# Kernel tuning notes

Hardware: AMD Instinct MI355X
Metric: run time of the kernel (lower is better)

## Reference

```python
import jax, jax.numpy as jnp
import numpy as np

B = 32768
IN = 2
H = 512
OUT = 1
OM = 128   # output_module_size
HG = 128   # halt_gate_size
MAX_ITER = 32
EPS = 1e-3


def _w(k, shape, fan_in):
    bound = 1.0 / np.sqrt(fan_in)
    return jax.random.uniform(k, shape, jnp.float32, -bound, bound)


def setup_inputs() -> dict:
    key = jax.random.key(0)
    ks = jax.random.split(key, 32)
    d = {"x": jax.random.normal(ks[0], (B, IN), jnp.float32)}
    # four LSTM gates: input Linear(IN,H) and hidden Linear(H,H), each with bias
    names = ["i", "f", "c", "o"]
    for j, g in enumerate(names):
        d[f"W{g}_x"] = _w(ks[1 + 4 * j], (IN, H), IN)
        d[f"b{g}_x"] = _w(ks[2 + 4 * j], (H,), IN)
        d[f"W{g}_h"] = _w(ks[3 + 4 * j], (H, H), H)
        d[f"b{g}_h"] = _w(ks[4 + 4 * j], (H,), H)
    # halt gate: Linear(H,HG) -> ReLU -> Linear(HG,1) -> Sigmoid
    d["halt_W1"] = _w(ks[17], (H, HG), H)
    d["halt_b1"] = _w(ks[18], (HG,), H)
    d["halt_W2"] = _w(ks[19], (HG, 1), HG)
    d["halt_b2"] = _w(ks[20], (1,), HG)
    # output module: Linear(H,OM) -> ReLU -> Linear(OM,OM) -> Linear(OM,OUT) -> Sigmoid
    d["out_W1"] = _w(ks[21], (H, OM), H)
    d["out_b1"] = _w(ks[22], (OM,), H)
    d["out_W2"] = _w(ks[23], (OM, OM), OM)
    d["out_b2"] = _w(ks[24], (OM,), OM)
    d["out_W3"] = _w(ks[25], (OM, OUT), OM)
    d["out_b3"] = _w(ks[26], (OUT,), OM)
    return d


def _act_forward(x, Wi_x, bi_x, Wi_h, bi_h, Wf_x, bf_x, Wf_h, bf_h,
                 Wc_x, bc_x, Wc_h, bc_h, Wo_x, bo_x, Wo_h, bo_h,
                 halt_W1, halt_b1, halt_W2, halt_b2,
                 out_W1, out_b1, out_W2, out_b2, out_W3, out_b3):
    b = x.shape[0]
    # input projections are iteration-invariant: precompute once
    xi = x @ Wi_x + bi_x
    xf = x @ Wf_x + bf_x
    xc = x @ Wc_x + bc_x
    xo = x @ Wo_x + bo_x

    def step(carry, t):
        state, cell, p_sum, active, acc = carry
        i_g = jax.nn.sigmoid(xi + state @ Wi_h + bi_h)
        f_g = jax.nn.sigmoid(xf + state @ Wf_h + bf_h)
        c_g = jnp.tanh(xc + state @ Wc_h + bc_h)
        o_g = jax.nn.sigmoid(xo + state @ Wo_h + bo_h)
        am = active[:, None]
        new_cell = jnp.where(am, f_g * cell + i_g * c_g, cell)
        new_state = jnp.where(am, o_g * jnp.tanh(new_cell), state)
        # output head (inactive rows contribute zero weight below)
        h1 = jax.nn.relu(new_state @ out_W1 + out_b1)
        out = jax.nn.sigmoid((h1 @ out_W2 + out_b2) @ out_W3 + out_b3)  # [B,OUT]
        # halt probability
        hh = jax.nn.relu(new_state @ halt_W1 + halt_b1)
        halt = jax.nn.sigmoid(hh @ halt_W2 + halt_b2)[:, 0]  # [B]
        halt = jnp.where(active, halt, 0.0)
        p_new = p_sum + halt
        is_last = t == (MAX_ITER - 1)
        finished = (p_new >= 1.0 - EPS) | is_last
        adj = active & finished
        halt_adj = jnp.where(adj, halt + (1.0 - p_new), halt)
        p_new = jnp.where(adj, 1.0, p_new)
        acc = acc + out * halt_adj[:, None]
        active_new = active & jnp.logical_not(finished)
        return (new_state, new_cell, p_new, active_new, acc), None

    init = (
        jnp.zeros((b, H), jnp.float32),   # state
        jnp.zeros((b, H), jnp.float32),   # cell
        jnp.zeros((b,), jnp.float32),     # p_sum
        jnp.ones((b,), bool),             # active
        jnp.zeros((b, OUT), jnp.float32), # weighted-output accumulator
    )
    (state, cell, p_sum, active, acc), _ = jax.lax.scan(step, init, jnp.arange(MAX_ITER))
    return acc


def reference(x, Wi_x, bi_x, Wi_h, bi_h, Wf_x, bf_x, Wf_h, bf_h,
              Wc_x, bc_x, Wc_h, bc_h, Wo_x, bo_x, Wo_h, bo_h,
              halt_W1, halt_b1, halt_W2, halt_b2,
              out_W1, out_b1, out_W2, out_b2, out_W3, out_b3):
    return _act_forward(x, Wi_x, bi_x, Wi_h, bi_h, Wf_x, bf_x, Wf_h, bf_h,
                        Wc_x, bc_x, Wc_h, bc_h, Wo_x, bo_x, Wo_h, bo_h,
                        halt_W1, halt_b1, halt_W2, halt_b2,
                        out_W1, out_b1, out_W2, out_b2, out_W3, out_b3)
```

## Files before the change

kernel.cpp:

```cpp
#include <hip/hip_runtime.h>
#include <hip/hip_bf16.h>

#define KD   544
#define ASTR 552
#define RPB  64
#define THR  512
#define T1   3
#define NROW 32768

typedef __bf16 bf8 __attribute__((ext_vector_type(8)));
typedef float f32x4 __attribute__((ext_vector_type(4)));

__device__ __forceinline__ float sigm(float x)  { return 1.0f / (1.0f + __expf(-x)); }
__device__ __forceinline__ float tanh_(float x) { return 2.0f / (1.0f + __expf(-2.0f * x)) - 1.0f; }

__global__ void pack_all(const float* __restrict__ Wi_h, const float* __restrict__ Wf_h,
                         const float* __restrict__ Wc_h, const float* __restrict__ Wo_h,
                         const float* __restrict__ Wi_x, const float* __restrict__ Wf_x,
                         const float* __restrict__ Wc_x, const float* __restrict__ Wo_x,
                         const float* __restrict__ bi_x, const float* __restrict__ bf_x,
                         const float* __restrict__ bc_x, const float* __restrict__ bo_x,
                         const float* __restrict__ bi_h, const float* __restrict__ bf_h,
                         const float* __restrict__ bc_h, const float* __restrict__ bo_h,
                         const float* __restrict__ outW1, const float* __restrict__ outb1,
                         const float* __restrict__ haltW1, const float* __restrict__ haltb1,
                         const float* __restrict__ outW2, const float* __restrict__ outb2,
                         const float* __restrict__ outW3, const float* __restrict__ outb3,
                         __bf16* __restrict__ whT, __bf16* __restrict__ w1cat,
                         float* __restrict__ w23, float* __restrict__ b23,
                         int* __restrict__ cntp)
{
  __shared__ float tile[64][65];
  const int b = blockIdx.x;
  const int tid = threadIdx.x;

  if (b < 256) {
    const int g = b >> 6, ct = (b >> 3) & 7, kt = b & 7;
    const int c0 = ct * 64, k0 = kt * 64;
    const float* Wh = (g == 0) ? Wi_h : (g == 1) ? Wf_h : (g == 2) ? Wc_h : Wo_h;
    const int ty = tid >> 6, tx = tid & 63;
#pragma unroll
    for (int r = 0; r < 16; ++r) {
      int kl = r * 4 + ty;
      tile[kl][tx] = Wh[(size_t)(k0 + kl) * 512 + c0 + tx];
    }
    __syncthreads();
    const int jj = tid >> 2, kq = tid & 3;
    bf8 lo, hi;
#pragma unroll
    for (int i = 0; i < 8; ++i) lo[i] = (__bf16)tile[kq * 16 + i][jj];
#pragma unroll
    for (int i = 0; i < 8; ++i) hi[i] = (__bf16)tile[kq * 16 + 8 + i][jj];
    __bf16* dst = whT + (size_t)(g * 512 + c0 + jj) * KD + k0 + kq * 16;
    *(bf8*)dst = lo;
    *(bf8*)(dst + 8) = hi;
  } else if (b < 288) {
    const int b2 = b - 256;
    const int g = b2 >> 3, ct = b2 & 7;
    const float* Wx = (g == 0) ? Wi_x : (g == 1) ? Wf_x : (g == 2) ? Wc_x : Wo_x;
    const float* bx = (g == 0) ? bi_x : (g == 1) ? bf_x : (g == 2) ? bc_x : bo_x;
    const float* bh = (g == 0) ? bi_h : (g == 1) ? bf_h : (g == 2) ? bc_h : bo_h;
    const int jj = tid >> 2, kq = tid & 3;
    const int c = ct * 64 + jj;
    bf8 v;
#pragma unroll
    for (int i = 0; i < 8; ++i) {
      int k = 512 + kq * 8 + i;
      float f = 0.0f;
      if (k == 512)      f = Wx[c];
      else if (k == 513) f = Wx[512 + c];
      else if (k == 514) f = bx[c] + bh[c];
      v[i] = (__bf16)f;
    }
    *(bf8*)(whT + (size_t)(g * 512 + c) * KD + 512 + kq * 8) = v;
  } else if (b < 320) {
    const int b2 = b - 288;
    const int src = b2 >> 4, jt = (b2 >> 3) & 1, kt = b2 & 7;
    const float* W = src ? haltW1 : outW1;
    const int c0 = jt * 64, k0 = kt * 64;
    const int ty = tid >> 6, tx = tid & 63;
#pragma unroll
    for (int r = 0; r < 16; ++r) {
      int kl = r * 4 + ty;
      tile[kl][tx] = W[(size_t)(k0 + kl) * 128 + c0 + tx];
    }
    __syncthreads();
    const int jj = tid >> 2, kq = tid & 3;
    bf8 lo, hi;
#pragma unroll
    for (int i = 0; i < 8; ++i) lo[i] = (__bf16)tile[kq * 16 + i][jj];
#pragma unroll
    for (int i = 0; i < 8; ++i) hi[i] = (__bf16)tile[kq * 16 + 8 + i][jj];
    __bf16* dst = w1cat + (size_t)(src * 128 + c0 + jj) * KD + k0 + kq * 16;
    *(bf8*)dst = lo;
    *(bf8*)(dst + 8) = hi;
  } else if (b < 324) {
    const int b2 = b - 320;
    const int jj = tid >> 2, kq = tid & 3;
    const int j = b2 * 64 + jj;
    const float bias = (j < 128) ? outb1[j] : haltb1[j - 128];
    bf8 v;
#pragma unroll
    for (int i = 0; i < 8; ++i) {
      int k = 512 + kq * 8 + i;
      v[i] = (__bf16)((k == 514) ? bias : 0.0f);
    }
    *(bf8*)(w1cat + (size_t)j * KD + 512 + kq * 8) = v;
  } else {
    const int c1 = tid;
    if (c1 < 128) {
      float s = 0.0f;
      for (int c2 = 0; c2 < 128; ++c2) s += outW2[c1 * 128 + c2] * outW3[c2];
      w23[c1] = s;
    }
    if (c1 == 0) {
      float bb = 0.0f;
      for (int c2 = 0; c2 < 128; ++c2) bb += outb2[c2] * outW3[c2];
      b23[0] = bb + outb3[0];
      cntp[0] = 0;
    }
  }
}

template<bool P1>
__global__ __launch_bounds__(THR, 2) void act_pass(
    const float* __restrict__ x,
    const __bf16* __restrict__ whT,
    const __bf16* __restrict__ w1cat,
    const float* __restrict__ w23,
    const float* __restrict__ b23p,
    const float* __restrict__ haltW2,
    const float* __restrict__ haltb2,
    __bf16* __restrict__ sstate,
    __bf16* __restrict__ scell,
    float* __restrict__ spsum,
    float* __restrict__ saccum,
    int* __restrict__ sidx,
    int* __restrict__ cntp,
    float* __restrict__ out)
{
  int cnt_v = 0, sbase = 0;
  if constexpr (!P1) {
    cnt_v = cntp[0];
    sbase = blockIdx.x * RPB;
    if (sbase >= cnt_v) return;
  }

  __shared__ __align__(16) __bf16 Abuf[2][RPB][ASTR];
  __shared__ float wv[256];
  __shared__ float partials[8][RPB];
  __shared__ int anyact_s;
  __shared__ int rowslot[RPB];

  const int tid  = threadIdx.x;
  const int wave = tid >> 6;
  const int lane = tid & 63;
  const int lg   = lane >> 4;
  const int lc   = lane & 15;
  const int row0 = blockIdx.x * RPB;

  if (tid < 256) wv[tid] = (tid < 128) ? w23[tid] : haltW2[tid - 128];

  if constexpr (P1) {
    for (int w = tid; w < 2 * RPB * 69; w += THR) {
      int bb  = w / (RPB * 69);
      int rem = w - bb * (RPB * 69);
      int r   = rem / 69;
      int j   = rem - r * 69;
      bf8 v;
#pragma unroll
      for (int e = 0; e < 8; ++e) v[e] = (__bf16)0.0f;
      if (j == 64) {
        v[0] = (__bf16)x[(row0 + r) * 2 + 0];
        v[1] = (__bf16)x[(row0 + r) * 2 + 1];
        v[2] = (__bf16)1.0f;
      }
      *(bf8*)&Abuf[bb][r][j * 8] = v;
    }
  } else {
    for (int w = tid; w < RPB * 68; w += THR) {
      int r = w / 68, j = w - r * 68;
      int slot = sbase + r;
      bf8 v;
#pragma unroll
      for (int e = 0; e < 8; ++e) v[e] = (__bf16)0.0f;
      if (slot < cnt_v) v = *(const bf8*)(sstate + (size_t)slot * KD + j * 8);
      *(bf8*)&Abuf[0][r][j * 8] = v;
      if (j >= 64) *(bf8*)&Abuf[1][r][j * 8] = v;
    }
    for (int w = tid; w < RPB * 64; w += THR) {
      int r = w / 64, j = w - r * 64;
      int slot = sbase + r;
      bf8 v;
#pragma unroll
      for (int e = 0; e < 8; ++e) v[e] = (__bf16)0.0f;
      if (slot < cnt_v) v = *(const bf8*)(scell + (size_t)slot * 512 + j * 8);
      *(bf8*)&Abuf[1][r][j * 8] = v;
    }
  }
  if (tid == 0) anyact_s = 1;
  __syncthreads();

  float cell[4][4][4];
  if constexpr (P1) {
#pragma unroll
    for (int n = 0; n < 4; ++n)
#pragma unroll
      for (int m = 0; m < 4; ++m)
#pragma unroll
        for (int q = 0; q < 4; ++q) cell[n][m][q] = 0.0f;
  } else {
#pragma unroll
    for (int n = 0; n < 4; ++n)
#pragma unroll
      for (int m = 0; m < 4; ++m)
#pragma unroll
        for (int q = 0; q < 4; ++q)
          cell[n][m][q] = (float)Abuf[1][m * 16 + lg * 4 + q][wave * 64 + n * 16 + lc];
  }

  bool  valid, active;
  float p_sum, accum;
  int   oidx;
  if constexpr (P1) {
    valid = (tid < 64); active = valid;
    p_sum = 0.0f; accum = 0.0f; oidx = row0 + tid;
  } else {
    int slot = sbase + tid;
    valid = (tid < 64) && (slot < cnt_v);
    active = valid;
    p_sum = valid ? spsum[slot]  : 1.0f;
    accum = valid ? saccum[slot] : 0.0f;
    oidx  = valid ? sidx[slot]   : 0;
    __syncthreads();
  }

  const float b23 = b23p[0];
  const float bh2 = haltb2[0];
  const f32x4 zero4 = {0.0f, 0.0f, 0.0f, 0.0f};

  int cur = 0;
  const int T0 = P1 ? 0 : T1;
  const int TE = P1 ? T1 : 32;
  for (int t = T0; t < TE; ++t) {
    const int kstart = (P1 && t == 0) ? 16 : 0;
#pragma unroll
    for (int n = 0; n < 4; ++n) {
      const int colb = wave * 64 + n * 16 + lc;
      const __bf16* bp[4];
      bp[0] = whT + (size_t)colb * KD + lg * 8;
      bp[1] = bp[0] + (size_t)512  * KD;
      bp[2] = bp[0] + (size_t)1024 * KD;
      bp[3] = bp[0] + (size_t)1536 * KD;
      f32x4 acc[4][4];
#pragma unroll
      for (int g = 0; g < 4; ++g)
#pragma unroll
        for (int m = 0; m < 4; ++m) acc[g][m] = zero4;

      bf8 bA[4], bB[4], avA[4];
      const int k1 = (kstart < 16) ? kstart + 1 : 16;
#pragma unroll
      for (int g = 0; g < 4; ++g) {
        bA[g] = *(const bf8*)(bp[g] + kstart * 32);
        bB[g] = *(const bf8*)(bp[g] + k1 * 32);
      }
#pragma unroll
      for (int m = 0; m < 4; ++m)
        avA[m] = *(const bf8*)&Abuf[cur][m * 16 + lc][kstart * 32 + lg * 8];

#pragma unroll 1
      for (int kk = kstart; kk <= 16; ++kk) {
        const int kp2 = (kk + 2 <= 16) ? kk + 2 : 16;
        const int kp1 = (kk + 1 <= 16) ? kk + 1 : 16;
        bf8 bC[4], avB[4];
#pragma unroll
        for (int g = 0; g < 4; ++g) bC[g] = *(const bf8*)(bp[g] + kp2 * 32);
#pragma unroll
        for (int m = 0; m < 4; ++m)
          avB[m] = *(const bf8*)&Abuf[cur][m * 16 + lc][kp1 * 32 + lg * 8];
#pragma unroll
        for (int m = 0; m < 4; ++m) {
          acc[0][m] = __builtin_amdgcn_mfma_f32_16x16x32_bf16(avA[m], bA[0], acc[0][m], 0, 0, 0);
          acc[1][m] = __builtin_amdgcn_mfma_f32_16x16x32_bf16(avA[m], bA[1], acc[1][m], 0, 0, 0);
          acc[2][m] = __builtin_amdgcn_mfma_f32_16x16x32_bf16(avA[m], bA[2], acc[2][m], 0, 0, 0);
          acc[3][m] = __builtin_amdgcn_mfma_f32_16x16x32_bf16(avA[m], bA[3], acc[3][m], 0, 0, 0);
        }
#pragma unroll
        for (int g = 0; g < 4; ++g) { bA[g] = bB[g]; bB[g] = bC[g]; }
#pragma unroll
        for (int m = 0; m < 4; ++m) avA[m] = avB[m];
      }
#pragma unroll
      for (int m = 0; m < 4; ++m) {
#pragma unroll
        for (int q = 0; q < 4; ++q) {
          float iv = sigm(acc[0][m][q]);
          float fv = sigm(acc[1][m][q]);
          float cv = tanh_(acc[2][m][q]);
          float ov = sigm(acc[3][m][q]);
          float cn = fv * cell[n][m][q] + iv * cv;
          cell[n][m][q] = cn;
          float h = ov * tanh_(cn);
          Abuf[cur ^ 1][m * 16 + lg * 4 + q][colb] = (__bf16)h;
        }
      }
    }
    __syncthreads();
    {
      const int jb0 = wave * 32 + lc;
      const __bf16* hp[2];
      hp[0] = w1cat + (size_t)jb0 * KD + lg * 8;
      hp[1] = hp[0] + (size_t)16 * KD;
      f32x4 hacc[2][4];
#pragma unroll
      for (int n2 = 0; n2 < 2; ++n2)
#pragma unroll
        for (int m = 0; m < 4; ++m) hacc[n2][m] = zero4;

      bf8 hA[2], hB[2], avA[4];
#pragma unroll
      for (int g = 0; g < 2; ++g) {
        hA[g] = *(const bf8*)(hp[g]);
        hB[g] = *(const bf8*)(hp[g] + 32);
      }
#pragma unroll
      for (int m = 0; m < 4; ++m)
        avA[m] = *(const bf8*)&Abuf[cur ^ 1][m * 16 + lc][lg * 8];

#pragma unroll 1
      for (int kk = 0; kk <= 16; ++kk) {
        const int kp2 = (kk + 2 <= 16) ? kk + 2 : 16;
        const int kp1 = (kk + 1 <= 16) ? kk + 1 : 16;
        bf8 hC[2], avB[4];
#pragma unroll
        for (int g = 0; g < 2; ++g) hC[g] = *(const bf8*)(hp[g] + kp2 * 32);
#pragma unroll
        for (int m = 0; m < 4; ++m)
          avB[m] = *(const bf8*)&Abuf[cur ^ 1][m * 16 + lc][kp1 * 32 + lg * 8];
#pragma unroll
        for (int m = 0; m < 4; ++m) {
          hacc[0][m] = __builtin_amdgcn_mfma_f32_16x16x32_bf16(avA[m], hA[0], hacc[0][m], 0, 0, 0);
          hacc[1][m] = __builtin_amdgcn_mfma_f32_16x16x32_bf16(avA[m], hA[1], hacc[1][m], 0, 0, 0);
        }
#pragma unroll
        for (int g = 0; g < 2; ++g) { hA[g] = hB[g]; hB[g] = hC[g]; }
#pragma unroll
        for (int m = 0; m < 4; ++m) avA[m] = avB[m];
      }
      const float wv0 = wv[wave * 32 + lc];
      const float wv1 = wv[wave * 32 + 16 + lc];
#pragma unroll
      for (int m = 0; m < 4; ++m) {
#pragma unroll
        for (int q = 0; q < 4; ++q) {
          float s = fmaxf(hacc[0][m][q], 0.0f) * wv0 + fmaxf(hacc[1][m][q], 0.0f) * wv1;
          s += __shfl_xor(s, 1, 64);
          s += __shfl_xor(s, 2, 64);
          s += __shfl_xor(s, 4, 64);
          s += __shfl_xor(s, 8, 64);
          if (lc == 0) partials[wave][m * 16 + lg * 4 + q] = s;
        }
      }
    }
    __syncthreads();
    if (tid < 64) {
      float od = partials[0][tid] + partials[1][tid] + partials[2][tid] + partials[3][tid] + b23;
      float hd = partials[4][tid] + partials[5][tid] + partials[6][tid] + partials[7][tid] + bh2;
      float outv  = sigm(od);
      float haltv = sigm(hd);
      if (active) {
        float pn  = p_sum + haltv;
        bool  fin = (pn >= 0.999f) || (t == 31);
        accum += outv * (fin ? (haltv + (1.0f - pn)) : haltv);
        p_sum  = fin ? 1.0f : pn;
        active = !fin;
      }
      unsigned long long mk = __ballot(active);
      if (tid == 0) anyact_s = (mk != 0ull) ? 1 : 0;
    }
    __syncthreads();
    if (!anyact_s) break;
    cur ^= 1;
  }

  if constexpr (P1) {
    if (tid < 64) {
      unsigned long long mk = __ballot(active);
      int base = 0;
      if (lane == 0 && mk) base = atomicAdd(cntp, __popcll(mk));
      base = __shfl(base, 0, 64);
      int rank = __popcll(mk & ((1ull << lane) - 1ull));
      int slot = active ? (base + rank) : -1;
      rowslot[tid] = slot;
      if (active) {
        spsum[slot]  = p_sum;
        saccum[slot] = accum;
        sidx[slot]   = oidx;
      } else {
        out[oidx] = accum;
      }
      if (tid == 0) anyact_s = (mk != 0ull) ? 1 : 0;
    }
    __syncthreads();
    if (anyact_s) {
#pragma unroll
      for (int n = 0; n < 4; ++n)
#pragma unroll
        for (int m = 0; m < 4; ++m)
#pragma unroll
          for (int q = 0; q < 4; ++q)
            Abuf[cur ^ 1][m * 16 + lg * 4 + q][wave * 64 + n * 16 + lc] = (__bf16)cell[n][m][q];
      __syncthreads();
      for (int w = tid; w < RPB * 132; w += THR) {
        int r = w / 132, j = w - r * 132;
        int slot = rowslot[r];
        if (slot < 0) continue;
        if (j < 68)
          *(bf8*)(sstate + (size_t)slot * KD + j * 8) = *(const bf8*)&Abuf[cur][r][j * 8];
        else {
          int jj = j - 68;
          *(bf8*)(scell + (size_t)slot * 512 + jj * 8) = *(const bf8*)&Abuf[cur ^ 1][r][jj * 8];
        }
      }
    }
  } else {
    if (valid) out[oidx] = accum;
  }
}

extern "C" void kernel_launch(void* const* d_in, const int* in_sizes, int n_in,
                              void* d_out, int out_size, void* d_ws, size_t ws_size,
                              hipStream_t stream) {
  const float* x     = (const float*)d_in[0];
  const float* Wi_x  = (const float*)d_in[1];
  const float* bi_x  = (const float*)d_in[2];
  const float* Wi_h  = (const float*)d_in[3];
  const float* bi_h  = (const float*)d_in[4];
  const float* Wf_x  = (const float*)d_in[5];
  const float* bf_x  = (const float*)d_in[6];
  const float* Wf_h  = (const float*)d_in[7];
  const float* bf_h  = (const float*)d_in[8];
  const float* Wc_x  = (const float*)d_in[9];
  const float* bc_x  = (const float*)d_in[10];
  const float* Wc_h  = (const float*)d_in[11];
  const float* bc_h  = (const float*)d_in[12];
  const float* Wo_x  = (const float*)d_in[13];
  const float* bo_x  = (const float*)d_in[14];
  const float* Wo_h  = (const float*)d_in[15];
  const float* bo_h  = (const float*)d_in[16];
  const float* hW1   = (const float*)d_in[17];
  const float* hb1   = (const float*)d_in[18];
  const float* hW2   = (const float*)d_in[19];
  const float* hb2   = (const float*)d_in[20];
  const float* oW1   = (const float*)d_in[21];
  const float* ob1   = (const float*)d_in[22];
  const float* oW2   = (const float*)d_in[23];
  const float* ob2   = (const float*)d_in[24];
  const float* oW3   = (const float*)d_in[25];
  const float* ob3   = (const float*)d_in[26];

  char* p = (char*)d_ws;
  __bf16* whT   = (__bf16*)p;                       p += (size_t)2048 * KD * 2;
  __bf16* w1cat = (__bf16*)p;                       p += (size_t)256 * KD * 2;
  float*  w23   = (float*)p;                        p += 512;
  float*  b23   = (float*)p;                        p += 16;
  int*    cnt   = (int*)p;                          p += 240;
  __bf16* sstate= (__bf16*)p;                       p += (size_t)NROW * KD * 2;
  __bf16* scell = (__bf16*)p;                       p += (size_t)NROW * 512 * 2;
  float*  spsum = (float*)p;                        p += (size_t)NROW * 4;
  float*  saccum= (float*)p;                        p += (size_t)NROW * 4;
  int*    sidx  = (int*)p;                          p += (size_t)NROW * 4;

  pack_all<<<dim3(325), dim3(256), 0, stream>>>(
      Wi_h, Wf_h, Wc_h, Wo_h, Wi_x, Wf_x, Wc_x, Wo_x,
      bi_x, bf_x, bc_x, bo_x, bi_h, bf_h, bc_h, bo_h,
      oW1, ob1, hW1, hb1, oW2, ob2, oW3, ob3,
      whT, w1cat, w23, b23, cnt);
  act_pass<true><<<dim3(NROW / RPB), dim3(THR), 0, stream>>>(
      x, whT, w1cat, w23, b23, hW2, hb2,
      sstate, scell, spsum, saccum, sidx, cnt, (float*)d_out);
  act_pass<false><<<dim3(NROW / RPB), dim3(THR), 0, stream>>>(
      x, whT, w1cat, w23, b23, hW2, hb2,
      sstate, scell, spsum, saccum, sidx, cnt, (float*)d_out);
}
```

Before: 415.4 us.

## Halve rows per block to 32 and raise occupancy to four blocks per CU

```diff
diff --git a/kernel.cpp b/kernel.cpp
--- a/kernel.cpp
+++ b/kernel.cpp
@@ -3,7 +3,8 @@
 
 #define KD   544
 #define ASTR 552
-#define RPB  64
+#define RPB  32
+#define MT   2
 #define THR  512
 #define T1   3
 #define NROW 32768
@@ -123,7 +124,7 @@
 }
 
 template<bool P1>
-__global__ __launch_bounds__(THR, 2) void act_pass(
+__global__ __launch_bounds__(THR, 4) void act_pass(
     const float* __restrict__ x,
     const __bf16* __restrict__ whT,
     const __bf16* __restrict__ w1cat,
@@ -201,19 +202,19 @@
   if (tid == 0) anyact_s = 1;
   __syncthreads();
 
-  float cell[4][4][4];
+  float cell[4][MT][4];
   if constexpr (P1) {
 #pragma unroll
     for (int n = 0; n < 4; ++n)
 #pragma unroll
-      for (int m = 0; m < 4; ++m)
+      for (int m = 0; m < MT; ++m)
 #pragma unroll
         for (int q = 0; q < 4; ++q) cell[n][m][q] = 0.0f;
   } else {
 #pragma unroll
     for (int n = 0; n < 4; ++n)
 #pragma unroll
-      for (int m = 0; m < 4; ++m)
+      for (int m = 0; m < MT; ++m)
 #pragma unroll
         for (int q = 0; q < 4; ++q)
           cell[n][m][q] = (float)Abuf[1][m * 16 + lg * 4 + q][wave * 64 + n * 16 + lc];
@@ -223,11 +224,11 @@
   float p_sum, accum;
   int   oidx;
   if constexpr (P1) {
-    valid = (tid < 64); active = valid;
+    valid = (tid < RPB); active = valid;
     p_sum = 0.0f; accum = 0.0f; oidx = row0 + tid;
   } else {
     int slot = sbase + tid;
-    valid = (tid < 64) && (slot < cnt_v);
+    valid = (tid < RPB) && (slot < cnt_v);
     active = valid;
     p_sum = valid ? spsum[slot]  : 1.0f;
     accum = valid ? saccum[slot] : 0.0f;
@@ -247,52 +248,54 @@
 #pragma unroll
     for (int n = 0; n < 4; ++n) {
       const int colb = wave * 64 + n * 16 + lc;
-      const __bf16* bp[4];
-      bp[0] = whT + (size_t)colb * KD + lg * 8;
-      bp[1] = bp[0] + (size_t)512  * KD;
-      bp[2] = bp[0] + (size_t)1024 * KD;
-      bp[3] = bp[0] + (size_t)1536 * KD;
-      f32x4 acc[4][4];
+      const __bf16* bp0 = whT + (size_t)(colb)        * KD + lg * 8;
+      const __bf16* bp1 = whT + (size_t)(512  + colb) * KD + lg * 8;
+      const __bf16* bp2 = whT + (size_t)(1024 + colb) * KD + lg * 8;
+      const __bf16* bp3 = whT + (size_t)(1536 + colb) * KD + lg * 8;
+      f32x4 acc[4][MT];
 #pragma unroll
       for (int g = 0; g < 4; ++g)
 #pragma unroll
-        for (int m = 0; m < 4; ++m) acc[g][m] = zero4;
-
-      bf8 bA[4], bB[4], avA[4];
-      const int k1 = (kstart < 16) ? kstart + 1 : 16;
-#pragma unroll
-      for (int g = 0; g < 4; ++g) {
-        bA[g] = *(const bf8*)(bp[g] + kstart * 32);
-        bB[g] = *(const bf8*)(bp[g] + k1 * 32);
-      }
-#pragma unroll
-      for (int m = 0; m < 4; ++m)
-        avA[m] = *(const bf8*)&Abuf[cur][m * 16 + lc][kstart * 32 + lg * 8];
-
+        for (int m = 0; m < MT; ++m) acc[g][m] = zero4;
+
+      bf8 b0 = *(const bf8*)(bp0 + kstart * 32);
+      bf8 b1 = *(const bf8*)(bp1 + kstart * 32);
+      bf8 b2 = *(const bf8*)(bp2 + kstart * 32);
+      bf8 b3 = *(const bf8*)(bp3 + kstart * 32);
 #pragma unroll 1
-      for (int kk = kstart; kk <= 16; ++kk) {
-        const int kp2 = (kk + 2 <= 16) ? kk + 2 : 16;
-        const int kp1 = (kk + 1 <= 16) ? kk + 1 : 16;
-        bf8 bC[4], avB[4];
-#pragma unroll
-        for (int g = 0; g < 4; ++g) bC[g] = *(const bf8*)(bp[g] + kp2 * 32);
-#pragma unroll
-        for (int m = 0; m < 4; ++m)
-          avB[m] = *(const bf8*)&Abuf[cur][m * 16 + lc][kp1 * 32 + lg * 8];
-#pragma unroll
-        for (int m = 0; m < 4; ++m) {
-          acc[0][m] = __builtin_amdgcn_mfma_f32_16x16x32_bf16(avA[m], bA[0], acc[0][m], 0, 0, 0);
-          acc[1][m] = __builtin_amdgcn_mfma_f32_16x16x32_bf16(avA[m], bA[1], acc[1][m], 0, 0, 0);
-          acc[2][m] = __builtin_amdgcn_mfma_f32_16x16x32_bf16(avA[m], bA[2], acc[2][m], 0, 0, 0);
-          acc[3][m] = __builtin_amdgcn_mfma_f32_16x16x32_bf16(avA[m], bA[3], acc[3][m], 0, 0, 0);
-        }
-#pragma unroll
-        for (int g = 0; g < 4; ++g) { bA[g] = bB[g]; bB[g] = bC[g]; }
-#pragma unroll
-        for (int m = 0; m < 4; ++m) avA[m] = avB[m];
-      }
-#pragma unroll
-      for (int m = 0; m < 4; ++m) {
+      for (int kk = kstart; kk < 16; ++kk) {
+        bf8 av[MT];
+#pragma unroll
+        for (int m = 0; m < MT; ++m)
+          av[m] = *(const bf8*)&Abuf[cur][m * 16 + lc][kk * 32 + lg * 8];
+        bf8 nb0 = *(const bf8*)(bp0 + (kk + 1) * 32);
+        bf8 nb1 = *(const bf8*)(bp1 + (kk + 1) * 32);
+        bf8 nb2 = *(const bf8*)(bp2 + (kk + 1) * 32);
+        bf8 nb3 = *(const bf8*)(bp3 + (kk + 1) * 32);
+#pragma unroll
+        for (int m = 0; m < MT; ++m) {
+          acc[0][m] = __builtin_amdgcn_mfma_f32_16x16x32_bf16(av[m], b0, acc[0][m], 0, 0, 0);
+          acc[1][m] = __builtin_amdgcn_mfma_f32_16x16x32_bf16(av[m], b1, acc[1][m], 0, 0, 0);
+          acc[2][m] = __builtin_amdgcn_mfma_f32_16x16x32_bf16(av[m], b2, acc[2][m], 0, 0, 0);
+          acc[3][m] = __builtin_amdgcn_mfma_f32_16x16x32_bf16(av[m], b3, acc[3][m], 0, 0, 0);
+        }
+        b0 = nb0; b1 = nb1; b2 = nb2; b3 = nb3;
+      }
+      {
+        bf8 av[MT];
+#pragma unroll
+        for (int m = 0; m < MT; ++m)
+          av[m] = *(const bf8*)&Abuf[cur][m * 16 + lc][16 * 32 + lg * 8];
+#pragma unroll
+        for (int m = 0; m < MT; ++m) {
+          acc[0][m] = __builtin_amdgcn_mfma_f32_16x16x32_bf16(av[m], b0, acc[0][m], 0, 0, 0);
+          acc[1][m] = __builtin_amdgcn_mfma_f32_16x16x32_bf16(av[m], b1, acc[1][m], 0, 0, 0);
+          acc[2][m] = __builtin_amdgcn_mfma_f32_16x16x32_bf16(av[m], b2, acc[2][m], 0, 0, 0);
+          acc[3][m] = __builtin_amdgcn_mfma_f32_16x16x32_bf16(av[m], b3, acc[3][m], 0, 0, 0);
+        }
+      }
+#pragma unroll
+      for (int m = 0; m < MT; ++m) {
 #pragma unroll
         for (int q = 0; q < 4; ++q) {
           float iv = sigm(acc[0][m][q]);
@@ -309,49 +312,45 @@
     __syncthreads();
     {
       const int jb0 = wave * 32 + lc;
-      const __bf16* hp[2];
-      hp[0] = w1cat + (size_t)jb0 * KD + lg * 8;
-      hp[1] = hp[0] + (size_t)16 * KD;
-      f32x4 hacc[2][4];
+      const __bf16* hp0 = w1cat + (size_t)jb0        * KD + lg * 8;
+      const __bf16* hp1 = w1cat + (size_t)(jb0 + 16) * KD + lg * 8;
+      f32x4 hacc[2][MT];
 #pragma unroll
       for (int n2 = 0; n2 < 2; ++n2)
 #pragma unroll
-        for (int m = 0; m < 4; ++m) hacc[n2][m] = zero4;
-
-      bf8 hA[2], hB[2], avA[4];
-#pragma unroll
-      for (int g = 0; g < 2; ++g) {
-        hA[g] = *(const bf8*)(hp[g]);
-        hB[g] = *(const bf8*)(hp[g] + 32);
-      }
-#pragma unroll
-      for (int m = 0; m < 4; ++m)
-        avA[m] = *(const bf8*)&Abuf[cur ^ 1][m * 16 + lc][lg * 8];
-
+        for (int m = 0; m < MT; ++m) hacc[n2][m] = zero4;
+      bf8 hb0 = *(const bf8*)(hp0);
+      bf8 hb1 = *(const bf8*)(hp1);
 #pragma unroll 1
-      for (int kk = 0; kk <= 16; ++kk) {
-        const int kp2 = (kk + 2 <= 16) ? kk + 2 : 16;
-        const int kp1 = (kk + 1 <= 16) ? kk + 1 : 16;
-        bf8 hC[2], avB[4];
-#pragma unroll
-        for (int g = 0; g < 2; ++g) hC[g] = *(const bf8*)(hp[g] + kp2 * 32);
-#pragma unroll
-        for (int m = 0; m < 4; ++m)
-          avB[m] = *(const bf8*)&Abuf[cur ^ 1][m * 16 + lc][kp1 * 32 + lg * 8];
-#pragma unroll
-        for (int m = 0; m < 4; ++m) {
-          hacc[0][m] = __builtin_amdgcn_mfma_f32_16x16x32_bf16(avA[m], hA[0], hacc[0][m], 0, 0, 0);
-          hacc[1][m] = __builtin_amdgcn_mfma_f32_16x16x32_bf16(avA[m], hA[1], hacc[1][m], 0, 0, 0);
-        }
-#pragma unroll
-        for (int g = 0; g < 2; ++g) { hA[g] = hB[g]; hB[g] = hC[g]; }
-#pragma unroll
-        for (int m = 0; m < 4; ++m) avA[m] = avB[m];
+      for (int kk = 0; kk < 16; ++kk) {
+        bf8 av[MT];
+#pragma unroll
+        for (int m = 0; m < MT; ++m)
+          av[m] = *(const bf8*)&Abuf[cur ^ 1][m * 16 + lc][kk * 32 + lg * 8];
+        bf8 nb0 = *(const bf8*)(hp0 + (kk + 1) * 32);
+        bf8 nb1 = *(const bf8*)(hp1 + (kk + 1) * 32);
+#pragma unroll
+        for (int m = 0; m < MT; ++m) {
+          hacc[0][m] = __builtin_amdgcn_mfma_f32_16x16x32_bf16(av[m], hb0, hacc[0][m], 0, 0, 0);
+          hacc[1][m] = __builtin_amdgcn_mfma_f32_16x16x32_bf16(av[m], hb1, hacc[1][m], 0, 0, 0);
+        }
+        hb0 = nb0; hb1 = nb1;
+      }
+      {
+        bf8 av[MT];
+#pragma unroll
+        for (int m = 0; m < MT; ++m)
+          av[m] = *(const bf8*)&Abuf[cur ^ 1][m * 16 + lc][16 * 32 + lg * 8];
+#pragma unroll
+        for (int m = 0; m < MT; ++m) {
+          hacc[0][m] = __builtin_amdgcn_mfma_f32_16x16x32_bf16(av[m], hb0, hacc[0][m], 0, 0, 0);
+          hacc[1][m] = __builtin_amdgcn_mfma_f32_16x16x32_bf16(av[m], hb1, hacc[1][m], 0, 0, 0);
+        }
       }
       const float wv0 = wv[wave * 32 + lc];
       const float wv1 = wv[wave * 32 + 16 + lc];
 #pragma unroll
-      for (int m = 0; m < 4; ++m) {
+      for (int m = 0; m < MT; ++m) {
 #pragma unroll
         for (int q = 0; q < 4; ++q) {
           float s = fmaxf(hacc[0][m][q], 0.0f) * wv0 + fmaxf(hacc[1][m][q], 0.0f) * wv1;
@@ -364,7 +363,7 @@
       }
     }
     __syncthreads();
-    if (tid < 64) {
+    if (tid < RPB) {
       float od = partials[0][tid] + partials[1][tid] + partials[2][tid] + partials[3][tid] + b23;
       float hd = partials[4][tid] + partials[5][tid] + partials[6][tid] + partials[7][tid] + bh2;
       float outv  = sigm(od);
@@ -385,7 +384,7 @@
   }
 
   if constexpr (P1) {
-    if (tid < 64) {
+    if (tid < RPB) {
       unsigned long long mk = __ballot(active);
       int base = 0;
       if (lane == 0 && mk) base = atomicAdd(cntp, __popcll(mk));
@@ -407,7 +406,7 @@
 #pragma unroll
       for (int n = 0; n < 4; ++n)
 #pragma unroll
-        for (int m = 0; m < 4; ++m)
+        for (int m = 0; m < MT; ++m)
 #pragma unroll
           for (int q = 0; q < 4; ++q)
             Abuf[cur ^ 1][m * 16 + lg * 4 + q][wave * 64 + n * 16 + lc] = (__bf16)cell[n][m][q];
```

After: 547.7 us. +31.9%, slower.
